# Performance work log

Measured on AMD Instinct MI355X. Metric: run time of the kernel, lower is better.

The kernel has to match this reference:

```python
import math
import jax
import jax.numpy as jnp
import numpy as np

WH, WW = 8, 8
DIM, NUM_HEADS = 768, 24
CPB_HIDDEN = 512


def _rel_tables(Wh, Ww):
    # relative_position_index: (N, N) int, values in [0, (2Wh-1)*(2Ww-1))
    coords = np.stack(np.meshgrid(np.arange(Wh), np.arange(Ww), indexing='ij')).reshape(2, -1)
    rel = coords[:, :, None] - coords[:, None, :]          # (2, N, N)
    rel = rel.transpose(1, 2, 0).astype(np.int64)          # (N, N, 2)
    rel[:, :, 0] += Wh - 1
    rel[:, :, 1] += Ww - 1
    rel[:, :, 0] *= 2 * Ww - 1
    idx = rel.sum(-1)                                      # (N, N)
    # relative_coords_table: ((2Wh-1)*(2Ww-1), 2), log-spaced CPB coords
    rch = np.arange(-(Wh - 1), Wh, dtype=np.float32)
    rcw = np.arange(-(Ww - 1), Ww, dtype=np.float32)
    table = np.stack(np.meshgrid(rch, rcw, indexing='ij')).transpose(1, 2, 0).reshape(-1, 2)
    table[:, 0] /= max(Wh - 1, 1)
    table[:, 1] /= max(Ww - 1, 1)
    table *= 8.0
    table = np.sign(table) * np.log2(np.abs(table) + 1.0) / math.log2(8.0)
    return idx.astype(np.int32), table.astype(np.float32)


def setup_inputs() -> dict:
    key = jax.random.key(0)
    ks = jax.random.split(key, 8)
    B_, N, C = 1024, WH * WW, DIM
    idx, table = _rel_tables(WH, WW)
    return {
        'x': jax.random.normal(ks[0], (B_, N, C), dtype=jnp.float32),
        'qkv_w': jax.random.normal(ks[1], (C, 3 * C), dtype=jnp.float32) * 0.02,
        'qkv_b': jnp.zeros((3 * C,), dtype=jnp.float32),
        'proj_w': jax.random.normal(ks[2], (C, C), dtype=jnp.float32) * 0.02,
        'proj_b': jnp.zeros((C,), dtype=jnp.float32),
        'cpb_w1': jax.random.normal(ks[3], (2, CPB_HIDDEN), dtype=jnp.float32) * 0.1,
        'cpb_b1': jnp.zeros((CPB_HIDDEN,), dtype=jnp.float32),
        'cpb_w2': jax.random.normal(ks[4], (CPB_HIDDEN, NUM_HEADS), dtype=jnp.float32) * 0.05,
        'logit_scale': jnp.full((NUM_HEADS, 1, 1), math.log(10.0), dtype=jnp.float32),
        'rel_coords_table': jnp.asarray(table),
        'rel_pos_index': jnp.asarray(idx),
    }


def reference(x, qkv_w, qkv_b, proj_w, proj_b, cpb_w1, cpb_b1, cpb_w2,
              logit_scale, rel_coords_table, rel_pos_index):
    B_, N, C = x.shape
    H = logit_scale.shape[0]
    hd = C // H
    qkv = (x @ qkv_w + qkv_b).reshape(B_, N, 3, H, hd).transpose(2, 0, 3, 1, 4)
    q, k, v = qkv[0], qkv[1], qkv[2]                        # (B_, H, N, hd)
    # cosine attention: L2-normalize q, k (eps as in F.normalize)
    q = q / jnp.maximum(jnp.linalg.norm(q, axis=-1, keepdims=True), 1e-12)
    k = k / jnp.maximum(jnp.linalg.norm(k, axis=-1, keepdims=True), 1e-12)
    ls = jnp.exp(jnp.minimum(logit_scale, math.log(1.0 / 0.01)))  # (H,1,1)
    q = q * ls
    # CPB bias: MLP over rel coords table, gather by relative_position_index
    bias_table = jnp.maximum(rel_coords_table @ cpb_w1 + cpb_b1, 0.0) @ cpb_w2  # (T, H)
    bias = bias_table[rel_pos_index.reshape(-1)].reshape(N, N, H).transpose(2, 0, 1)[None]  # (1,H,N,N)
    attn = jnp.einsum('bhnd,bhmd->bhnm', q, k) + bias      # scale = 1.0
    attn = jax.nn.softmax(attn, axis=-1)
    out = jnp.einsum('bhnm,bhmd->bhnd', attn, v)
    out = out.transpose(0, 2, 1, 3).reshape(B_, N, C)
    return out @ proj_w + proj_b
```

## Files before the change

### kernel.cpp

```cpp
#include <hip/hip_runtime.h>
#include <hip/hip_bf16.h>

typedef __bf16 bf16_t;
typedef __bf16 bf16x8 __attribute__((ext_vector_type(8)));
typedef float f32x4 __attribute__((ext_vector_type(4)));

static __device__ __forceinline__ f32x4 mfma16(bf16x8 a, bf16x8 b, f32x4 c) {
  return __builtin_amdgcn_mfma_f32_16x16x32_bf16(a, b, c, 0, 0, 0);
}

static __device__ __forceinline__ void gload16(const void* g, void* l) {
  __builtin_amdgcn_global_load_lds(
      (const __attribute__((address_space(1))) void*)g,
      (__attribute__((address_space(3))) void*)l, 16, 0, 0);
}

#define BAR() __builtin_amdgcn_s_barrier()
#define SCHED0() __builtin_amdgcn_sched_barrier(0)
#define MEMFENCE() asm volatile("" ::: "memory")
#define BARF() do { BAR(); MEMFENCE(); SCHED0(); } while (0)
#define WAITVM4() do { asm volatile("s_waitcnt vmcnt(4)" ::: "memory"); SCHED0(); } while (0)
#define WAITVM0() do { asm volatile("s_waitcnt vmcnt(0)" ::: "memory"); SCHED0(); } while (0)
#define WAITLGKM0() do { asm volatile("s_waitcnt lgkmcnt(0)" ::: "memory"); SCHED0(); } while (0)
#define SP1 __builtin_amdgcn_s_setprio(1)
#define SP0 __builtin_amdgcn_s_setprio(0)

__global__ __launch_bounds__(256) void prep_kernel(
    const float* __restrict__ x, bf16_t* __restrict__ xb,
    const float* __restrict__ qkv_w, bf16_t* __restrict__ wTq,
    const float* __restrict__ proj_w, bf16_t* __restrict__ wTp,
    const float* __restrict__ table, const float* __restrict__ w1,
    const float* __restrict__ b1, const float* __restrict__ w2,
    float* __restrict__ bias_table) {
  __shared__ __align__(16) char sm[4352];
  int blk = blockIdx.x;
  int tid = threadIdx.x;
  if (blk < 2048) {
    const int n8 = 6291456, stride = 2048 * 256;
    for (int i = blk * 256 + tid; i < n8; i += stride) {
      float4 a = ((const float4*)x)[2 * i];
      float4 b = ((const float4*)x)[2 * i + 1];
      bf16x8 w = {(bf16_t)a.x, (bf16_t)a.y, (bf16_t)a.z, (bf16_t)a.w,
                  (bf16_t)b.x, (bf16_t)b.y, (bf16_t)b.z, (bf16_t)b.w};
      ((bf16x8*)xb)[i] = w;
    }
    return;
  }
  if (blk < 4352) {
    const float* W;
    bf16_t* WT;
    int K = 768, N, r;
    if (blk < 3776) { W = qkv_w; WT = wTq; N = 2304; r = blk - 2048; }
    else            { W = proj_w; WT = wTp; N = 768;  r = blk - 3776; }
    int nbx = N / 32;
    int n0 = (r % nbx) * 32, k0 = (r / nbx) * 32;
    float (*tile)[33] = (float(*)[33])sm;
    int tx = tid & 31, ty = tid >> 5;
#pragma unroll
    for (int i = 0; i < 32; i += 8)
      tile[ty + i][tx] = W[(size_t)(k0 + ty + i) * N + n0 + tx];
    __syncthreads();
#pragma unroll
    for (int i = 0; i < 32; i += 8)
      WT[(size_t)(n0 + ty + i) * K + k0 + tx] = (bf16_t)tile[tx][ty + i];
    return;
  }
  {
    float* hbuf = (float*)sm;
    int t = blk - 4352;
    float c0 = table[2 * t], c1 = table[2 * t + 1];
    for (int u = tid; u < 512; u += 256) {
      float h = c0 * w1[u] + c1 * w1[512 + u] + b1[u];
      hbuf[u] = h > 0.f ? h : 0.f;
    }
    __syncthreads();
    int wave = tid >> 6, lane = tid & 63;
    for (int hh = wave * 6; hh < wave * 6 + 6; ++hh) {
      float s = 0.f;
      for (int jj = lane; jj < 512; jj += 64) s += hbuf[jj] * w2[jj * 24 + hh];
#pragma unroll
      for (int off = 32; off > 0; off >>= 1) s += __shfl_down(s, off, 64);
      if (lane == 0) bias_table[t * 24 + hh] = s;
    }
  }
}

__global__ __launch_bounds__(256) void bias_expand_kernel(
    const float* __restrict__ bias_table, const int* __restrict__ idx,
    float* __restrict__ bias) {
  int h = blockIdx.x;
  for (int nm = threadIdx.x; nm < 4096; nm += 256)
    bias[h * 4096 + nm] = bias_table[idx[nm] * 24 + h];
}

template <int EPI, int NCOLS, int K>
__global__ __launch_bounds__(512, 2) void gemm_kernel(
    const bf16_t* __restrict__ A, const bf16_t* __restrict__ BT,
    const float* __restrict__ bias, void* __restrict__ outp) {
  constexpr int NT = NCOLS / 256;
  constexpr int Kb = K * 2;
  constexpr int nk = K / 64;
  constexpr int nIt = nk / 2;
  __shared__ __align__(16) char lds[131072];
  int tid = threadIdx.x;
  int wave = tid >> 6, lane = tid & 63;
  int wm = wave >> 2, wn = wave & 3;
  int cpx = gridDim.x >> 3;
  int wg = (blockIdx.x & 7) * cpx + (blockIdx.x >> 3);
  int mt = wg / NT, nt = wg % NT;
  int m0 = mt * 256, n0 = nt * 256;

  int srow = tid >> 3;
  int sbc = ((tid & 7) << 4) ^ ((srow & 7) << 4);
  const char* Ag = (const char*)A + (size_t)(m0 + srow) * Kb + sbc;
  const char* Bg = (const char*)BT + (size_t)(n0 + srow) * Kb + sbc;
  char* Al = lds + tid * 16;
  char* Bl = lds + 65536 + tid * 16;

#define ST_A(B_, H_, KT_)                                                     \
  do {                                                                        \
    gload16(Ag + (size_t)((H_) * 128) * Kb + (KT_) * 128,                     \
            Al + (B_) * 32768 + (H_) * 16384);                                \
    gload16(Ag + (size_t)((H_) * 128 + 64) * Kb + (KT_) * 128,                \
            Al + (B_) * 32768 + (H_) * 16384 + 8192);                         \
  } while (0)
#define ST_B(B_, H_, KT_)                                                     \
  do {                                                                        \
    gload16(Bg + (size_t)((H_) * 128) * Kb + (KT_) * 128,                     \
            Bl + (B_) * 32768 + (H_) * 16384);                                \
    gload16(Bg + (size_t)((H_) * 128 + 64) * Kb + (KT_) * 128,                \
            Bl + (B_) * 32768 + (H_) * 16384 + 8192);                         \
  } while (0)

  int r15 = lane & 15, hi = lane >> 4;
  int swz = (lane & 7) << 4;
  int c0 = (hi << 4) ^ swz;
  int c1 = (64 | (hi << 4)) ^ swz;
  const char* aBase = lds + wm * 16384 + r15 * 128;
  const char* bBase = lds + 65536 + (wn >> 1) * 16384 + (wn & 1) * 8192 + r15 * 128;

#define RD_B8(B_)                                                             \
  do {                                                                        \
    _Pragma("unroll") for (int nc = 0; nc < 4; ++nc) {                        \
      bfr[nc][0] = *(const bf16x8*)(bBase + (B_) * 32768 + nc * 2048 + c0);   \
      bfr[nc][1] = *(const bf16x8*)(bBase + (B_) * 32768 + nc * 2048 + c1);   \
    }                                                                         \
  } while (0)
#define RD_A4(B_, MRLO, C_)                                                   \
  do {                                                                        \
    _Pragma("unroll") for (int m_ = 0; m_ < 4; ++m_)                          \
        af[m_] = *(const bf16x8*)(aBase + (B_) * 32768 + ((MRLO) + m_) * 2048 + (C_)); \
  } while (0)
#define MF16(MRLO, KKI)                                                       \
  do {                                                                        \
    _Pragma("unroll") for (int m_ = 0; m_ < 4; ++m_)                          \
        _Pragma("unroll") for (int nc = 0; nc < 4; ++nc)                      \
            acc[(MRLO) + m_][nc] =                                            \
        mfma16(af[m_], bfr[nc][KKI], acc[(MRLO) + m_][nc]);                   \
  } while (0)

  f32x4 acc[8][4] = {};
  ST_B(0, 0, 0); ST_B(0, 1, 0);
  ST_A(0, 0, 0); ST_A(0, 1, 0);
  ST_B(1, 0, 1); ST_B(1, 1, 1);
  WAITVM4();
  BARF();

  for (int it = 0; it < nIt - 1; ++it) {
    int T = 2 * it;
    bf16x8 af[4], bfr[4][2];
    RD_B8(0); RD_A4(0, 0, c0);
    ST_A(1, 0, T + 1); ST_A(1, 1, T + 1);
    BAR(); WAITLGKM0();
    SP1; MF16(0, 0); SP0;
    BARF();
    RD_A4(0, 4, c0);
    ST_B(0, 0, T + 2);
    BAR(); WAITLGKM0();
    SP1; MF16(4, 0); SP0;
    BARF();
    RD_A4(0, 0, c1);
    ST_B(0, 1, T + 2);
    BAR(); WAITLGKM0();
    SP1; MF16(0, 1); SP0;
    BARF();
    RD_A4(0, 4, c1);
    BAR(); WAITLGKM0();
    SP1; MF16(4, 1); SP0;
    WAITVM4();
    BARF();
    RD_B8(1); RD_A4(1, 0, c0);
    ST_A(0, 0, T + 2);
    BAR(); WAITLGKM0();
    SP1; MF16(0, 0); SP0;
    BARF();
    RD_A4(1, 4, c0);
    ST_A(0, 1, T + 2);
    BAR(); WAITLGKM0();
    SP1; MF16(4, 0); SP0;
    BARF();
    RD_A4(1, 0, c1);
    ST_B(1, 0, T + 3);
    BAR(); WAITLGKM0();
    SP1; MF16(0, 1); SP0;
    BARF();
    RD_A4(1, 4, c1);
    ST_B(1, 1, T + 3);
    BAR(); WAITLGKM0();
    SP1; MF16(4, 1); SP0;
    WAITVM4();
    BARF();
  }
  {
    bf16x8 af[4], bfr[4][2];
    RD_B8(0); RD_A4(0, 0, c0);
    ST_A(1, 0, nk - 1); ST_A(1, 1, nk - 1);
    BAR(); WAITLGKM0();
    SP1; MF16(0, 0); SP0;
    BARF();
    RD_A4(0, 4, c0);
    BAR(); WAITLGKM0();
    SP1; MF16(4, 0); SP0;
    BARF();
    RD_A4(0, 0, c1);
    BAR(); WAITLGKM0();
    SP1; MF16(0, 1); SP0;
    BARF();
    RD_A4(0, 4, c1);
    BAR(); WAITLGKM0();
    SP1; MF16(4, 1); SP0;
    WAITVM0();
    BARF();
    RD_B8(1); RD_A4(1, 0, c0);
    BAR(); WAITLGKM0();
    SP1; MF16(0, 0); SP0;
    BARF();
    RD_A4(1, 4, c0);
    BAR(); WAITLGKM0();
    SP1; MF16(4, 0); SP0;
    BARF();
    RD_A4(1, 0, c1);
    BAR(); WAITLGKM0();
    SP1; MF16(0, 1); SP0;
    BARF();
    RD_A4(1, 4, c1);
    BAR(); WAITLGKM0();
    SP1; MF16(4, 1); SP0;
  }

  int hi4 = hi * 4;
  if constexpr (EPI == 0) {
    bf16_t* out = (bf16_t*)outp;
    int sidx = n0 / 768;
#pragma unroll
    for (int mr = 0; mr < 8; ++mr)
#pragma unroll
      for (int nc = 0; nc < 4; ++nc) {
        int gcol = n0 + wn * 64 + nc * 16 + r15;
        int within = gcol - sidx * 768;
        int h = within >> 5, d = within & 31;
        float bv = bias[gcol];
#pragma unroll
        for (int j = 0; j < 4; ++j) {
          int grow = m0 + wm * 128 + mr * 16 + hi4 + j;
          int bwin = grow >> 6, nn = grow & 63;
          size_t off = ((((size_t)sidx * 1024 + bwin) * 24 + h) * 64 + nn) * 32 + d;
          out[off] = (bf16_t)(acc[mr][nc][j] + bv);
        }
      }
  } else {
    float* out = (float*)outp;
#pragma unroll
    for (int mr = 0; mr < 8; ++mr)
#pragma unroll
      for (int nc = 0; nc < 4; ++nc) {
        int gcol = n0 + wn * 64 + nc * 16 + r15;
        float bv = bias[gcol];
#pragma unroll
        for (int j = 0; j < 4; ++j) {
          int grow = m0 + wm * 128 + mr * 16 + hi4 + j;
          out[(size_t)grow * NCOLS + gcol] = acc[mr][nc][j] + bv;
        }
      }
  }
#undef ST_A
#undef ST_B
#undef RD_B8
#undef RD_A4
#undef MF16
}

__global__ __launch_bounds__(64) void attn_kernel(
    const bf16_t* __restrict__ qkv, const float* __restrict__ bias,
    const float* __restrict__ logit_scale, bf16_t* __restrict__ attn_out) {
  __shared__ __align__(16) char smem[13824];
  bf16_t (*qs)[40] = (bf16_t(*)[40])smem;
  bf16_t (*kk)[40] = (bf16_t(*)[40])(smem + 5120);
  bf16_t (*ps)[72] = (bf16_t(*)[72])smem;
  bf16_t (*vT)[72] = (bf16_t(*)[72])(smem + 9216);
  int h = blockIdx.x >> 10;
  int b = blockIdx.x & 1023;
  int lane = threadIdx.x;
  float ls = __expf(fminf(logit_scale[h], 4.6051701859880914f));
  size_t base = ((size_t)b * 24 + h) * 2048;
  const bf16_t* qrow = qkv + base + lane * 32;
  const bf16_t* krow = qkv + (size_t)50331648 + base + lane * 32;
  const bf16_t* vrow = qkv + (size_t)100663296 + base + lane * 32;
  bf16x8 vreg[4];
#pragma unroll
  for (int i = 0; i < 4; ++i) vreg[i] = *(const bf16x8*)(vrow + i * 8);
  {
    bf16x8 r[4];
#pragma unroll
    for (int i = 0; i < 4; ++i) r[i] = *(const bf16x8*)(qrow + i * 8);
    float f[32], sq = 0.f;
#pragma unroll
    for (int i = 0; i < 4; ++i)
#pragma unroll
      for (int j = 0; j < 8; ++j) { float x = (float)r[i][j]; f[i * 8 + j] = x; sq += x * x; }
    float sc = ls / fmaxf(sqrtf(sq), 1e-12f);
#pragma unroll
    for (int i = 0; i < 4; ++i) {
      bf16x8 w;
#pragma unroll
      for (int j = 0; j < 8; ++j) w[j] = (bf16_t)(f[i * 8 + j] * sc);
      *(bf16x8*)&qs[lane][i * 8] = w;
    }
  }
  {
    bf16x8 r[4];
#pragma unroll
    for (int i = 0; i < 4; ++i) r[i] = *(const bf16x8*)(krow + i * 8);
    float f[32], sq = 0.f;
#pragma unroll
    for (int i = 0; i < 4; ++i)
#pragma unroll
      for (int j = 0; j < 8; ++j) { float x = (float)r[i][j]; f[i * 8 + j] = x; sq += x * x; }
    float sc = 1.f / fmaxf(sqrtf(sq), 1e-12f);
#pragma unroll
    for (int i = 0; i < 4; ++i) {
      bf16x8 w;
#pragma unroll
      for (int j = 0; j < 8; ++j) w[j] = (bf16_t)(f[i * 8 + j] * sc);
      *(bf16x8*)&kk[lane][i * 8] = w;
    }
  }
  __syncthreads();
  f32x4 sacc[4][4] = {};
  {
    bf16x8 qa[4], kb[4];
#pragma unroll
    for (int mr = 0; mr < 4; ++mr)
      qa[mr] = *(bf16x8*)&qs[mr * 16 + (lane & 15)][(lane >> 4) * 8];
#pragma unroll
    for (int nc = 0; nc < 4; ++nc)
      kb[nc] = *(bf16x8*)&kk[nc * 16 + (lane & 15)][(lane >> 4) * 8];
    SP1;
#pragma unroll
    for (int mr = 0; mr < 4; ++mr)
#pragma unroll
      for (int nc = 0; nc < 4; ++nc)
        sacc[mr][nc] = mfma16(qa[mr], kb[nc], sacc[mr][nc]);
    SP0;
  }
  __syncthreads();
  {
#pragma unroll
    for (int i = 0; i < 4; ++i)
#pragma unroll
      for (int j = 0; j < 8; ++j) vT[i * 8 + j][lane] = vreg[i][j];
  }
  const float* bh = bias + h * 4096;
  int hi4 = (lane >> 4) * 4;
  float rsum[4][4];
#pragma unroll
  for (int mr = 0; mr < 4; ++mr)
#pragma unroll
    for (int j = 0; j < 4; ++j) {
      int r = mr * 16 + hi4 + j;
      float v0 = __expf(sacc[mr][0][j] + bh[r * 64 + 0 + (lane & 15)]);
      float v1 = __expf(sacc[mr][1][j] + bh[r * 64 + 16 + (lane & 15)]);
      float v2 = __expf(sacc[mr][2][j] + bh[r * 64 + 32 + (lane & 15)]);
      float v3 = __expf(sacc[mr][3][j] + bh[r * 64 + 48 + (lane & 15)]);
      float sum = v0 + v1 + v2 + v3;
#pragma unroll
      for (int off = 1; off < 16; off <<= 1) sum += __shfl_xor(sum, off, 64);
      rsum[mr][j] = sum;
      ps[r][0 + (lane & 15)] = (bf16_t)v0;
      ps[r][16 + (lane & 15)] = (bf16_t)v1;
      ps[r][32 + (lane & 15)] = (bf16_t)v2;
      ps[r][48 + (lane & 15)] = (bf16_t)v3;
    }
  __syncthreads();
  f32x4 oacc[4][2] = {};
#pragma unroll
  for (int ks_ = 0; ks_ < 2; ++ks_) {
    bf16x8 pa[4], vb[2];
#pragma unroll
    for (int mr = 0; mr < 4; ++mr)
      pa[mr] = *(bf16x8*)&ps[mr * 16 + (lane & 15)][ks_ * 32 + (lane >> 4) * 8];
#pragma unroll
    for (int c2 = 0; c2 < 2; ++c2)
      vb[c2] = *(bf16x8*)&vT[c2 * 16 + (lane & 15)][ks_ * 32 + (lane >> 4) * 8];
    SP1;
#pragma unroll
    for (int mr = 0; mr < 4; ++mr)
#pragma unroll
      for (int c2 = 0; c2 < 2; ++c2)
        oacc[mr][c2] = mfma16(pa[mr], vb[c2], oacc[mr][c2]);
    SP0;
  }
#pragma unroll
  for (int mr = 0; mr < 4; ++mr) {
    float rinv[4];
#pragma unroll
    for (int j = 0; j < 4; ++j) rinv[j] = 1.f / rsum[mr][j];
#pragma unroll
    for (int c2 = 0; c2 < 2; ++c2) {
      int d = c2 * 16 + (lane & 15);
#pragma unroll
      for (int j = 0; j < 4; ++j) {
        int r = mr * 16 + hi4 + j;
        attn_out[((size_t)b * 64 + r) * 768 + h * 32 + d] =
            (bf16_t)(oacc[mr][c2][j] * rinv[j]);
      }
    }
  }
}

extern "C" void kernel_launch(void* const* d_in, const int* in_sizes, int n_in,
                              void* d_out, int out_size, void* d_ws, size_t ws_size,
                              hipStream_t stream) {
  const float* x = (const float*)d_in[0];
  const float* qkv_w = (const float*)d_in[1];
  const float* qkv_b = (const float*)d_in[2];
  const float* proj_w = (const float*)d_in[3];
  const float* proj_b = (const float*)d_in[4];
  const float* cpb_w1 = (const float*)d_in[5];
  const float* cpb_b1 = (const float*)d_in[6];
  const float* cpb_w2 = (const float*)d_in[7];
  const float* logit_scale = (const float*)d_in[8];
  const float* rel_tab = (const float*)d_in[9];
  const int* rel_idx = (const int*)d_in[10];

  char* ws = (char*)d_ws;
  float* bias_table = (float*)ws;
  float* bias = (float*)(ws + 32768);
  bf16_t* wTq = (bf16_t*)(ws + 425984);
  bf16_t* wTp = (bf16_t*)(ws + 3964928);
  bf16_t* qkv = (bf16_t*)(ws + 5144576);
  bf16_t* xb = (bf16_t*)(ws + 307134464);
  bf16_t* attn = xb;

  prep_kernel<<<4577, 256, 0, stream>>>(x, xb, qkv_w, wTq, proj_w, wTp,
                                        rel_tab, cpb_w1, cpb_b1, cpb_w2,
                                        bias_table);
  bias_expand_kernel<<<24, 256, 0, stream>>>(bias_table, rel_idx, bias);
  gemm_kernel<0, 2304, 768><<<2304, 512, 0, stream>>>(xb, wTq, qkv_b, qkv);
  attn_kernel<<<24576, 64, 0, stream>>>(qkv, bias, logit_scale, attn);
  gemm_kernel<1, 768, 768><<<768, 512, 0, stream>>>(attn, wTp, proj_b, d_out);
}
```

Measured before the change: 535.7 us.

## Fuse CPB bias expansion into prep kernel and XOR-swizzle attention LDS

Removes the separate bias_expand launch: each of 24 prep blocks now computes one head's bias table column for all 225 coordinates in registers and scatters it directly through rel_pos_index into the expanded bias buffer. The attention kernel replaces padded P and V^T LDS arrays with 128-byte rows using an XOR swizzle, shrinking shared memory and aiming to avoid bank conflicts on the transposed V writes and fragment reads. The bias MLP is now serial per thread (512-step loop), which could lengthen the tail of the prep kernel.

```diff
diff --git a/kernel.cpp b/kernel.cpp
--- a/kernel.cpp
+++ b/kernel.cpp
@@ -31,7 +31,7 @@
     const float* __restrict__ proj_w, bf16_t* __restrict__ wTp,
     const float* __restrict__ table, const float* __restrict__ w1,
     const float* __restrict__ b1, const float* __restrict__ w2,
-    float* __restrict__ bias_table) {
+    const int* __restrict__ rel_idx, float* __restrict__ bias) {
   __shared__ __align__(16) char sm[4352];
   int blk = blockIdx.x;
   int tid = threadIdx.x;
@@ -66,31 +66,21 @@
     return;
   }
   {
-    float* hbuf = (float*)sm;
-    int t = blk - 4352;
-    float c0 = table[2 * t], c1 = table[2 * t + 1];
-    for (int u = tid; u < 512; u += 256) {
-      float h = c0 * w1[u] + c1 * w1[512 + u] + b1[u];
-      hbuf[u] = h > 0.f ? h : 0.f;
+    float* sbuf = (float*)sm;
+    int h = blk - 4352;
+    if (tid < 225) {
+      float c0 = table[2 * tid], c1 = table[2 * tid + 1];
+      float s = 0.f;
+      for (int j = 0; j < 512; ++j) {
+        float hh = c0 * w1[j] + c1 * w1[512 + j] + b1[j];
+        s += fmaxf(hh, 0.f) * w2[j * 24 + h];
+      }
+      sbuf[tid] = s;
     }
     __syncthreads();
-    int wave = tid >> 6, lane = tid & 63;
-    for (int hh = wave * 6; hh < wave * 6 + 6; ++hh) {
-      float s = 0.f;
-      for (int jj = lane; jj < 512; jj += 64) s += hbuf[jj] * w2[jj * 24 + hh];
-#pragma unroll
-      for (int off = 32; off > 0; off >>= 1) s += __shfl_down(s, off, 64);
-      if (lane == 0) bias_table[t * 24 + hh] = s;
-    }
-  }
-}
-
-__global__ __launch_bounds__(256) void bias_expand_kernel(
-    const float* __restrict__ bias_table, const int* __restrict__ idx,
-    float* __restrict__ bias) {
-  int h = blockIdx.x;
-  for (int nm = threadIdx.x; nm < 4096; nm += 256)
-    bias[h * 4096 + nm] = bias_table[idx[nm] * 24 + h];
+    for (int nm = tid; nm < 4096; nm += 256)
+      bias[h * 4096 + nm] = sbuf[rel_idx[nm]];
+  }
 }
 
 template <int EPI, int NCOLS, int K>
@@ -293,14 +283,13 @@
 __global__ __launch_bounds__(64) void attn_kernel(
     const bf16_t* __restrict__ qkv, const float* __restrict__ bias,
     const float* __restrict__ logit_scale, bf16_t* __restrict__ attn_out) {
-  __shared__ __align__(16) char smem[13824];
+  __shared__ __align__(16) char smem[12288];
   bf16_t (*qs)[40] = (bf16_t(*)[40])smem;
   bf16_t (*kk)[40] = (bf16_t(*)[40])(smem + 5120);
-  bf16_t (*ps)[72] = (bf16_t(*)[72])smem;
-  bf16_t (*vT)[72] = (bf16_t(*)[72])(smem + 9216);
   int h = blockIdx.x >> 10;
   int b = blockIdx.x & 1023;
   int lane = threadIdx.x;
+  int l15 = lane & 15, hi = lane >> 4;
   float ls = __expf(fminf(logit_scale[h], 4.6051701859880914f));
   size_t base = ((size_t)b * 24 + h) * 2048;
   const bf16_t* qrow = qkv + base + lane * 32;
@@ -351,10 +340,10 @@
     bf16x8 qa[4], kb[4];
 #pragma unroll
     for (int mr = 0; mr < 4; ++mr)
-      qa[mr] = *(bf16x8*)&qs[mr * 16 + (lane & 15)][(lane >> 4) * 8];
+      qa[mr] = *(bf16x8*)&qs[mr * 16 + l15][hi * 8];
 #pragma unroll
     for (int nc = 0; nc < 4; ++nc)
-      kb[nc] = *(bf16x8*)&kk[nc * 16 + (lane & 15)][(lane >> 4) * 8];
+      kb[nc] = *(bf16x8*)&kk[nc * 16 + l15][hi * 8];
     SP1;
 #pragma unroll
     for (int mr = 0; mr < 4; ++mr)
@@ -368,40 +357,50 @@
 #pragma unroll
     for (int i = 0; i < 4; ++i)
 #pragma unroll
-      for (int j = 0; j < 8; ++j) vT[i * 8 + j][lane] = vreg[i][j];
+      for (int j = 0; j < 8; ++j) {
+        int d = i * 8 + j;
+        *(bf16_t*)(smem + 8192 + (d << 7) + ((lane << 1) ^ ((d & 7) << 4))) =
+            vreg[i][j];
+      }
   }
   const float* bh = bias + h * 4096;
-  int hi4 = (lane >> 4) * 4;
+  int hi4 = hi * 4;
   float rsum[4][4];
 #pragma unroll
   for (int mr = 0; mr < 4; ++mr)
 #pragma unroll
     for (int j = 0; j < 4; ++j) {
       int r = mr * 16 + hi4 + j;
-      float v0 = __expf(sacc[mr][0][j] + bh[r * 64 + 0 + (lane & 15)]);
-      float v1 = __expf(sacc[mr][1][j] + bh[r * 64 + 16 + (lane & 15)]);
-      float v2 = __expf(sacc[mr][2][j] + bh[r * 64 + 32 + (lane & 15)]);
-      float v3 = __expf(sacc[mr][3][j] + bh[r * 64 + 48 + (lane & 15)]);
+      float v0 = __expf(sacc[mr][0][j] + bh[r * 64 + 0 + l15]);
+      float v1 = __expf(sacc[mr][1][j] + bh[r * 64 + 16 + l15]);
+      float v2 = __expf(sacc[mr][2][j] + bh[r * 64 + 32 + l15]);
+      float v3 = __expf(sacc[mr][3][j] + bh[r * 64 + 48 + l15]);
       float sum = v0 + v1 + v2 + v3;
 #pragma unroll
       for (int off = 1; off < 16; off <<= 1) sum += __shfl_xor(sum, off, 64);
       rsum[mr][j] = sum;
-      ps[r][0 + (lane & 15)] = (bf16_t)v0;
-      ps[r][16 + (lane & 15)] = (bf16_t)v1;
-      ps[r][32 + (lane & 15)] = (bf16_t)v2;
-      ps[r][48 + (lane & 15)] = (bf16_t)v3;
+      int rb = (r << 7), sw = (r & 7) << 4;
+      *(bf16_t*)(smem + rb + (((0 * 32) + (l15 << 1)) ^ sw)) = (bf16_t)v0;
+      *(bf16_t*)(smem + rb + (((1 * 32) + (l15 << 1)) ^ sw)) = (bf16_t)v1;
+      *(bf16_t*)(smem + rb + (((2 * 32) + (l15 << 1)) ^ sw)) = (bf16_t)v2;
+      *(bf16_t*)(smem + rb + (((3 * 32) + (l15 << 1)) ^ sw)) = (bf16_t)v3;
     }
   __syncthreads();
   f32x4 oacc[4][2] = {};
 #pragma unroll
   for (int ks_ = 0; ks_ < 2; ++ks_) {
     bf16x8 pa[4], vb[2];
-#pragma unroll
-    for (int mr = 0; mr < 4; ++mr)
-      pa[mr] = *(bf16x8*)&ps[mr * 16 + (lane & 15)][ks_ * 32 + (lane >> 4) * 8];
-#pragma unroll
-    for (int c2 = 0; c2 < 2; ++c2)
-      vb[c2] = *(bf16x8*)&vT[c2 * 16 + (lane & 15)][ks_ * 32 + (lane >> 4) * 8];
+    int cb = ks_ * 64 + hi * 16;
+#pragma unroll
+    for (int mr = 0; mr < 4; ++mr) {
+      int r = mr * 16 + l15;
+      pa[mr] = *(const bf16x8*)(smem + (r << 7) + (cb ^ ((r & 7) << 4)));
+    }
+#pragma unroll
+    for (int c2 = 0; c2 < 2; ++c2) {
+      int d = c2 * 16 + l15;
+      vb[c2] = *(const bf16x8*)(smem + 8192 + (d << 7) + (cb ^ ((d & 7) << 4)));
+    }
     SP1;
 #pragma unroll
     for (int mr = 0; mr < 4; ++mr)
@@ -417,7 +416,7 @@
     for (int j = 0; j < 4; ++j) rinv[j] = 1.f / rsum[mr][j];
 #pragma unroll
     for (int c2 = 0; c2 < 2; ++c2) {
-      int d = c2 * 16 + (lane & 15);
+      int d = c2 * 16 + l15;
 #pragma unroll
       for (int j = 0; j < 4; ++j) {
         int r = mr * 16 + hi4 + j;
@@ -444,7 +443,6 @@
   const int* rel_idx = (const int*)d_in[10];
 
   char* ws = (char*)d_ws;
-  float* bias_table = (float*)ws;
   float* bias = (float*)(ws + 32768);
   bf16_t* wTq = (bf16_t*)(ws + 425984);
   bf16_t* wTp = (bf16_t*)(ws + 3964928);
@@ -452,10 +450,9 @@
   bf16_t* xb = (bf16_t*)(ws + 307134464);
   bf16_t* attn = xb;
 
-  prep_kernel<<<4577, 256, 0, stream>>>(x, xb, qkv_w, wTq, proj_w, wTp,
+  prep_kernel<<<4376, 256, 0, stream>>>(x, xb, qkv_w, wTq, proj_w, wTp,
                                         rel_tab, cpb_w1, cpb_b1, cpb_w2,
-                                        bias_table);
-  bias_expand_kernel<<<24, 256, 0, stream>>>(bias_table, rel_idx, bias);
+                                        rel_idx, bias);
   gemm_kernel<0, 2304, 768><<<2304, 512, 0, stream>>>(xb, wTq, qkv_b, qkv);
   attn_kernel<<<24576, 64, 0, stream>>>(qkv, bias, logit_scale, attn);
   gemm_kernel<1, 768, 768><<<768, 512, 0, stream>>>(attn, wTp, proj_b, d_out);
```

New measurement: 597.4 us (median of 2 runs). 11.5% more time.
